# Optimization experiments

Measured on AMD Instinct MI355X. Metric: run time of the kernel, lower is better.

Reference implementation:

```python
import jax, jax.numpy as jnp
import numpy as np

B, L = 16, 512          # samples x tokens-per-sample
S = B * L               # total packed tokens
H, HKV, D = 16, 4, 128  # query heads, kv heads, head_dim
G = H // HKV            # GQA group size
HID = 2048
EPS = 1e-6


def rmsnorm(x, w):
    # Qwen2RMSNorm: fp32 variance, scale by weight
    v = jnp.mean(x.astype(jnp.float32) ** 2, axis=-1, keepdims=True)
    return (x.astype(jnp.float32) * jax.lax.rsqrt(v + EPS)).astype(x.dtype) * w


def rotate_half(x):
    x1, x2 = jnp.split(x, 2, axis=-1)
    return jnp.concatenate([-x2, x1], axis=-1)


def setup_inputs() -> dict:
    key = jax.random.key(0)
    ks = jax.random.split(key, 24)
    f = lambda k, shp, s=0.02: (jax.random.normal(k, shp, dtype=jnp.float32) * s)
    inp = {
        'packed_sequence_und': f(ks[0], (S // 2, HID), 1.0),
        'packed_sequence_gen': f(ks[1], (S // 2, HID), 1.0),
        # und tokens on even slots, gen on odd slots -> irregular scatter
        'packed_und_token_indexes': jnp.arange(0, S, 2, dtype=jnp.int32),
        'packed_gen_token_indexes': jnp.arange(1, S, 2, dtype=jnp.int32),
        # und-path projections (q/k/v have bias, o does not)
        'q_w': f(ks[2], (H * D, HID)), 'q_b': f(ks[3], (H * D,)),
        'k_w': f(ks[4], (HKV * D, HID)), 'k_b': f(ks[5], (HKV * D,)),
        'v_w': f(ks[6], (HKV * D, HID)), 'v_b': f(ks[7], (HKV * D,)),
        'o_w': f(ks[8], (HID, H * D)),
        # gen-path (moe_gen) projections
        'q_w_g': f(ks[9], (H * D, HID)), 'q_b_g': f(ks[10], (H * D,)),
        'k_w_g': f(ks[11], (HKV * D, HID)), 'k_b_g': f(ks[12], (HKV * D,)),
        'v_w_g': f(ks[13], (HKV * D, HID)), 'v_b_g': f(ks[14], (HKV * D,)),
        'o_w_g': f(ks[15], (HID, H * D)),
        # qk-norm weights
        'qn_w': jnp.ones((D,), jnp.float32), 'kn_w': jnp.ones((D,), jnp.float32),
        'qn_w_g': jnp.ones((D,), jnp.float32), 'kn_w_g': jnp.ones((D,), jnp.float32),
    }
    # RoPE cos/sin for packed positions (position resets per sample)
    pos = jnp.tile(jnp.arange(L, dtype=jnp.float32), B)            # [S]
    inv_freq = 1.0 / (1e6 ** (jnp.arange(0, D, 2, dtype=jnp.float32) / D))
    freqs = pos[:, None] * inv_freq[None, :]                       # [S, D/2]
    emb = jnp.concatenate([freqs, freqs], axis=-1)                 # [S, D]
    inp['packed_cos'] = jnp.cos(emb)
    inp['packed_sin'] = jnp.sin(emb)
    return inp


def reference(packed_sequence_und, packed_sequence_gen, packed_cos, packed_sin,
              packed_und_token_indexes, packed_gen_token_indexes,
              q_w, q_b, k_w, k_b, v_w, v_b, o_w,
              q_w_g, q_b_g, k_w_g, k_b_g, v_w_g, v_b_g, o_w_g,
              qn_w, kn_w, qn_w_g, kn_w_g):
    ui, gi = packed_und_token_indexes, packed_gen_token_indexes
    # dual-path QKV projection + index scatter into shared packed buffers
    q = jnp.zeros((S, H * D), jnp.float32)
    q = q.at[ui].set(packed_sequence_und @ q_w.T + q_b)
    q = q.at[gi].set(packed_sequence_gen @ q_w_g.T + q_b_g)
    k = jnp.zeros((S, HKV * D), jnp.float32)
    k = k.at[ui].set(packed_sequence_und @ k_w.T + k_b)
    k = k.at[gi].set(packed_sequence_gen @ k_w_g.T + k_b_g)
    v = jnp.zeros((S, HKV * D), jnp.float32)
    v = v.at[ui].set(packed_sequence_und @ v_w.T + v_b)
    v = v.at[gi].set(packed_sequence_gen @ v_w_g.T + v_b_g)

    q = q.reshape(S, H, D)
    k = k.reshape(S, HKV, D)
    v = v.reshape(S, HKV, D)

    # per-stream QK RMSNorm, scattered back
    q = jnp.zeros_like(q).at[ui].set(rmsnorm(q[ui], qn_w)).at[gi].set(rmsnorm(q[gi], qn_w_g))
    k = jnp.zeros_like(k).at[ui].set(rmsnorm(k[ui], kn_w)).at[gi].set(rmsnorm(k[gi], kn_w_g))

    # RoPE (unsqueeze_dim=1)
    cos, sin = packed_cos[:, None, :], packed_sin[:, None, :]
    q = q * cos + rotate_half(q) * sin
    k = k * cos + rotate_half(k) * sin

    # block-diagonal causal attention over packed samples (GQA)
    qb_ = q.reshape(B, L, HKV, G, D)
    kb_ = k.reshape(B, L, HKV, D)
    vb_ = v.reshape(B, L, HKV, D)
    scale = 1.0 / np.sqrt(D)
    scores = jnp.einsum('bqhgd,bkhd->bhgqk', qb_, kb_) * scale   # [B,HKV,G,L,L]
    causal = jnp.tril(jnp.ones((L, L), bool))
    scores = jnp.where(causal, scores, -jnp.inf)
    probs = jax.nn.softmax(scores, axis=-1)
    out = jnp.einsum('bhgqk,bkhd->bqhgd', probs, vb_)            # [B,L,HKV,G,D]
    out = out.reshape(S, H * D)

    out_und = out[ui] @ o_w.T
    out_gen = out[gi] @ o_w_g.T
    return (out_und, out_gen)
```

## Files before the change

### kernel.cpp

```cpp
#include <hip/hip_runtime.h>

typedef __bf16 bf16;
typedef __bf16 bf16x8 __attribute__((ext_vector_type(8)));
typedef float  f32x4  __attribute__((ext_vector_type(4)));

#define HALF   4096
#define S_TOT  8192
#define HID    2048
#define NH     16
#define NKV    4
#define DH     128
#define LSEQ   512

typedef const __attribute__((address_space(1))) void* as1_cvp;
typedef __attribute__((address_space(3))) void* as3_vp;

__device__ __forceinline__ void gl2lds16(const void* g, void* l) {
    __builtin_amdgcn_global_load_lds((as1_cvp)g, (as3_vp)l, 16, 0, 0);
}

struct CvtArgs {
    const float* src[10];
    bf16*        dst[10];
    int          n4[10];
};
__global__ __launch_bounds__(256) void k_convert_multi(CvtArgs a, int total4) {
    int i = blockIdx.x * 256 + threadIdx.x;
    if (i >= total4) return;
    int off = i;
    #pragma unroll
    for (int s = 0; s < 10; ++s) {
        if (off < a.n4[s]) {
            float4 v = ((const float4*)a.src[s])[off];
            union { bf16 b[4]; ushort4 u; } t;
            t.b[0] = (bf16)v.x; t.b[1] = (bf16)v.y; t.b[2] = (bf16)v.z; t.b[3] = (bf16)v.w;
            ((ushort4*)a.dst[s])[off] = t.u;
            return;
        }
        off -= a.n4[s];
    }
}

__global__ void k_invtyp(const int* __restrict__ ui, const int* __restrict__ gi,
                         int* __restrict__ it) {
    int t = blockIdx.x * 256 + threadIdx.x;
    if (t < HALF) { it[ui[t]] = t << 1; it[gi[t]] = (t << 1) | 1; }
}

__global__ __launch_bounds__(256) void k_gemm_qkv(
    const bf16* __restrict__ Xu, const bf16* __restrict__ Xg,
    const bf16* __restrict__ Wu, const bf16* __restrict__ Wg,
    const float* __restrict__ qbu, const float* __restrict__ kbu, const float* __restrict__ vbu,
    const float* __restrict__ qbg, const float* __restrict__ kbg, const float* __restrict__ vbg,
    const int* __restrict__ ui, const int* __restrict__ gi,
    bf16* __restrict__ qo, bf16* __restrict__ ko, bf16* __restrict__ vo)
{
    const int gen = blockIdx.z;
    const bf16* X = gen ? Xg : Xu;
    const bf16* W = gen ? Wg : Wu;
    const float* qb = gen ? qbg : qbu;
    const float* kb = gen ? kbg : kbu;
    const float* vb = gen ? vbg : vbu;
    const int* idx = gen ? gi : ui;

    __shared__ __align__(16) bf16 sA[128*32];
    __shared__ __align__(16) bf16 sB[128*32];

    const int tid = threadIdx.x;
    const int wave = tid >> 6, lane = tid & 63;
    const int lm = lane & 15, kq = lane >> 4;
    const int wm = wave >> 1, wn = wave & 1;
    const int m0 = blockIdx.y * 128, n0 = blockIdx.x * 128;

    f32x4 acc[4][4] = {};

    for (int k0 = 0; k0 < HID; k0 += 32) {
        __syncthreads();
        #pragma unroll
        for (int i = 0; i < 2; ++i) {
            const int g = i*4 + wave;
            const int c = g*64 + lane;
            const int row = c >> 2, col = c & 3;
            gl2lds16(X + (size_t)(m0+row)*HID + k0 + col*8, (char*)sA + (size_t)g*1024);
            gl2lds16(W + (size_t)(n0+row)*HID + k0 + col*8, (char*)sB + (size_t)g*1024);
        }
        __syncthreads();
        bf16x8 a[4], b[4];
        #pragma unroll
        for (int i = 0; i < 4; ++i) a[i] = *(const bf16x8*)&sA[(wm*64 + i*16 + lm)*32 + kq*8];
        #pragma unroll
        for (int j = 0; j < 4; ++j) b[j] = *(const bf16x8*)&sB[(wn*64 + j*16 + lm)*32 + kq*8];
        #pragma unroll
        for (int i = 0; i < 4; ++i)
            #pragma unroll
            for (int j = 0; j < 4; ++j)
                acc[i][j] = __builtin_amdgcn_mfma_f32_16x16x32_bf16(a[i], b[j], acc[i][j], 0, 0, 0);
    }

    #pragma unroll
    for (int i = 0; i < 4; ++i) {
        int srow[4];
        #pragma unroll
        for (int r = 0; r < 4; ++r) srow[r] = idx[m0 + wm*64 + i*16 + kq*4 + r];
        #pragma unroll
        for (int j = 0; j < 4; ++j) {
            const int o = n0 + wn*64 + j*16 + lm;
            bf16* dst; float bias; int off0, ld;
            if (o < 2048)      { dst = qo; ld = 2048; off0 = o;        bias = qb[o]; }
            else if (o < 2560) { dst = ko; ld = 512;  off0 = o - 2048; bias = kb[o-2048]; }
            else               { dst = vo; ld = 512;  off0 = o - 2560; bias = vb[o-2560]; }
            #pragma unroll
            for (int r = 0; r < 4; ++r)
                dst[(size_t)srow[r]*ld + off0] = (bf16)(acc[i][j][r] + bias);
        }
    }
}

__global__ __launch_bounds__(256) void k_norm_rope(
    bf16* __restrict__ qbuf, bf16* __restrict__ kbuf,
    const float* __restrict__ cosb, const float* __restrict__ sinb,
    const int* __restrict__ invtyp,
    const float* __restrict__ qnu, const float* __restrict__ qng,
    const float* __restrict__ knu, const float* __restrict__ kng)
{
    const int row = blockIdx.x * 4 + (threadIdx.x >> 6);
    const int lane = threadIdx.x & 63;
    const int s = row / (NH + NKV), hh = row % (NH + NKV);
    const int isg = invtyp[s] & 1;
    bf16* ptr; const float* w; float qs;
    if (hh < NH) { ptr = qbuf + (size_t)s*HID + hh*DH;           w = isg ? qng : qnu;
                   qs = 0.08838834764831845f * 1.4426950408889634f; }
    else         { ptr = kbuf + (size_t)s*(NKV*DH) + (hh-NH)*DH; w = isg ? kng : knu;
                   qs = 1.0f; }

    const unsigned u = *(const unsigned*)((const unsigned short*)ptr + 2*lane);
    const float f0 = __uint_as_float(u << 16);
    const float f1 = __uint_as_float(u & 0xffff0000u);
    float ss = f0*f0 + f1*f1;
    #pragma unroll
    for (int m = 32; m; m >>= 1) ss += __shfl_xor(ss, m, 64);
    const float r = rsqrtf(ss * (1.0f/128.0f) + 1e-6f);
    const float2 wv = *(const float2*)(w + 2*lane);
    const float xn0 = f0 * r * wv.x;
    const float xn1 = f1 * r * wv.y;
    const float po0 = __shfl_xor(xn0, 32, 64);
    const float po1 = __shfl_xor(xn1, 32, 64);
    const float2 c2 = *(const float2*)(cosb + (size_t)s*DH + 2*lane);
    const float2 s2 = *(const float2*)(sinb + (size_t)s*DH + 2*lane);
    const float sg = (lane < 32) ? -1.0f : 1.0f;
    const float o0 = (xn0 * c2.x + sg * po0 * s2.x) * qs;
    const float o1 = (xn1 * c2.y + sg * po1 * s2.y) * qs;
    union { unsigned short us[2]; unsigned u; } t;
    bf16 b0 = (bf16)o0, b1 = (bf16)o1;
    t.us[0] = *(unsigned short*)&b0; t.us[1] = *(unsigned short*)&b1;
    *(unsigned*)((unsigned short*)ptr + 2*lane) = t.u;
}

__global__ __launch_bounds__(256) void k_vtrans(const bf16* __restrict__ v, bf16* __restrict__ vt)
{
    __shared__ __align__(16) bf16 sT[64 * 132];
    const int kvh = blockIdx.y;
    const int s0 = blockIdx.x * 64;
    const int b = s0 >> 9;
    const int pos0 = s0 & 511;
    const int tid = threadIdx.x;

    #pragma unroll
    for (int i = 0; i < 4; ++i) {
        const int c = i*256 + tid;
        const int rowi = c >> 4, col8 = c & 15;
        const uint4 d = *(const uint4*)(v + (size_t)(s0 + rowi)*(NKV*DH) + kvh*DH + col8*8);
        uint2* lp = (uint2*)&sT[rowi*132 + col8*8];
        lp[0] = make_uint2(d.x, d.y);
        lp[1] = make_uint2(d.z, d.w);
    }
    __syncthreads();
    const int dd = tid >> 1, half = tid & 1;
    __align__(16) bf16 tmp[32];
    #pragma unroll
    for (int p = 0; p < 32; ++p) tmp[p] = sT[(half*32 + p)*132 + dd];
    bf16* dst = vt + ((size_t)(b*NKV + kvh)*DH + dd)*LSEQ + pos0 + half*32;
    #pragma unroll
    for (int q = 0; q < 8; ++q) ((ushort4*)dst)[q] = ((ushort4*)tmp)[q];
}

__global__ __launch_bounds__(256) void k_attn(
    const bf16* __restrict__ qbuf, const bf16* __restrict__ kbuf,
    const bf16* __restrict__ vt, const int* __restrict__ invtyp,
    bf16* __restrict__ aop_u, bf16* __restrict__ aop_g)
{
    __shared__ __align__(16) bf16 sK[2][64*128];
    __shared__ __align__(16) bf16 sV[2][128*64];
    __shared__ __align__(16) bf16 sP[4][16*72];

    const int qt = 7 - blockIdx.x;
    const int h = blockIdx.y, b = blockIdx.z;
    const int kvh = h >> 2;
    const int tid = threadIdx.x, wave = tid >> 6, lane = tid & 63;
    const int lm = lane & 15, kq = lane >> 4;
    const int q0 = qt * 64;

    bf16x8 qfrag[4];
    {
        const bf16* qp = qbuf + ((size_t)(b*LSEQ + q0 + wave*16 + lm))*HID + h*DH;
        #pragma unroll
        for (int ks = 0; ks < 4; ++ks)
            qfrag[ks] = *(const bf16x8*)(qp + ks*32 + kq*8);
    }

    const bf16* kbase = kbuf + ((size_t)(b*LSEQ))*(NKV*DH) + kvh*DH;
    const bf16* vbase = vt + ((size_t)(b*NKV + kvh)*DH)*LSEQ;

    f32x4 accO[8] = {};
    float lpart[4] = {0.f, 0.f, 0.f, 0.f};
    bf16* const sPw = &sP[wave][0];

    {
        const bf16* kp = kbase;
        const bf16* vp = vbase;
        #pragma unroll
        for (int i = 0; i < 4; ++i) {
            const int g = i*4 + wave;
            const int ch = g*64 + lane;
            { const int row = ch >> 4, cp = ch & 15;
              const int c = (cp & 8) | ((cp ^ row) & 7);
              gl2lds16(kp + (size_t)row*(NKV*DH) + c*8, (char*)&sK[0][0] + (size_t)g*1024); }
            { const int d = ch >> 3, cp = ch & 7;
              const int c = (cp ^ d) & 7;
              gl2lds16(vp + (size_t)d*LSEQ + c*8, (char*)&sV[0][0] + (size_t)g*1024); }
        }
    }

    for (int kt = 0; kt <= qt; ++kt) {
        const int cur = kt & 1;
        __syncthreads();

        if (kt < qt) {
            const bf16* kp = kbase + (size_t)((kt+1)*64)*(NKV*DH);
            const bf16* vp = vbase + (kt+1)*64;
            const int nxt = cur ^ 1;
            #pragma unroll
            for (int i = 0; i < 4; ++i) {
                const int g = i*4 + wave;
                const int ch = g*64 + lane;
                { const int row = ch >> 4, cp = ch & 15;
                  const int c = (cp & 8) | ((cp ^ row) & 7);
                  gl2lds16(kp + (size_t)row*(NKV*DH) + c*8, (char*)&sK[nxt][0] + (size_t)g*1024); }
                { const int d = ch >> 3, cp = ch & 7;
                  const int c = (cp ^ d) & 7;
                  gl2lds16(vp + (size_t)d*LSEQ + c*8, (char*)&sV[nxt][0] + (size_t)g*1024); }
            }
        }

        f32x4 s4[4] = {};
        #pragma unroll
        for (int ks = 0; ks < 4; ++ks) {
            const int cq = ks*4 + kq;
            const int cs = (cq & 8) | ((cq ^ lm) & 7);
            #pragma unroll
            for (int nt = 0; nt < 4; ++nt) {
                bf16x8 bk = *(const bf16x8*)&sK[cur][(nt*16 + lm)*128 + cs*8];
                s4[nt] = __builtin_amdgcn_mfma_f32_16x16x32_bf16(qfrag[ks], bk, s4[nt], 0, 0, 0);
            }
        }

        const bool diag = (kt == qt);
        #pragma unroll
        for (int r = 0; r < 4; ++r) {
            const int rloc = wave*16 + kq*4 + r;
            float v0 = s4[0][r], v1 = s4[1][r], v2 = s4[2][r], v3 = s4[3][r];
            if (diag) {
                if (lm      > rloc) v0 = -1e30f;
                if (lm + 16 > rloc) v1 = -1e30f;
                if (lm + 32 > rloc) v2 = -1e30f;
                if (lm + 48 > rloc) v3 = -1e30f;
            }
            const float p0 = exp2f(v0);
            const float p1 = exp2f(v1);
            const float p2 = exp2f(v2);
            const float p3 = exp2f(v3);
            lpart[r] += (p0 + p1) + (p2 + p3);
            const int prow = (kq*4 + r) * 72;
            sPw[prow + lm]      = (bf16)p0;
            sPw[prow + 16 + lm] = (bf16)p1;
            sPw[prow + 32 + lm] = (bf16)p2;
            sPw[prow + 48 + lm] = (bf16)p3;
        }

        #pragma unroll
        for (int pc = 0; pc < 2; ++pc) {
            bf16x8 ap = *(const bf16x8*)&sPw[lm*72 + pc*32 + kq*8];
            #pragma unroll
            for (int dt = 0; dt < 8; ++dt) {
                const int cv = (pc*4 + kq);
                const int cs = (cv ^ lm) & 7;
                bf16x8 bv = *(const bf16x8*)&sV[cur][(dt*16 + lm)*64 + cs*8];
                accO[dt] = __builtin_amdgcn_mfma_f32_16x16x32_bf16(ap, bv, accO[dt], 0, 0, 0);
            }
        }
    }

    #pragma unroll
    for (int r = 0; r < 4; ++r) {
        float l = lpart[r];
        l += __shfl_xor(l, 1, 64);
        l += __shfl_xor(l, 2, 64);
        l += __shfl_xor(l, 4, 64);
        l += __shfl_xor(l, 8, 64);
        const int srow = b*LSEQ + q0 + wave*16 + kq*4 + r;
        const int code = invtyp[srow];
        bf16* dst = (code & 1) ? aop_g : aop_u;
        const size_t off = (size_t)(code >> 1)*HID + h*DH;
        const float inv_l = 1.0f / l;
        #pragma unroll
        for (int dt = 0; dt < 8; ++dt)
            dst[off + dt*16 + lm] = (bf16)(accO[dt][r] * inv_l);
    }
}

__global__ __launch_bounds__(256) void k_gemm_out(
    const bf16* __restrict__ Au, const bf16* __restrict__ Ag,
    const bf16* __restrict__ Wu, const bf16* __restrict__ Wg,
    float* __restrict__ out)
{
    const int gen = blockIdx.z;
    const bf16* A = gen ? Ag : Au;
    const bf16* W = gen ? Wg : Wu;
    float* O = out + (size_t)gen * HALF * HID;

    __shared__ __align__(16) bf16 sA[128*32];
    __shared__ __align__(16) bf16 sB[128*32];

    const int tid = threadIdx.x;
    const int wave = tid >> 6, lane = tid & 63;
    const int lm = lane & 15, kq = lane >> 4;
    const int wm = wave >> 1, wn = wave & 1;
    const int m0 = blockIdx.y * 128, n0 = blockIdx.x * 128;

    f32x4 acc[4][4] = {};

    for (int k0 = 0; k0 < HID; k0 += 32) {
        __syncthreads();
        #pragma unroll
        for (int i = 0; i < 2; ++i) {
            const int g = i*4 + wave;
            const int c = g*64 + lane;
            const int row = c >> 2, col = c & 3;
            gl2lds16(A + (size_t)(m0+row)*HID + k0 + col*8, (char*)sA + (size_t)g*1024);
            gl2lds16(W + (size_t)(n0+row)*HID + k0 + col*8, (char*)sB + (size_t)g*1024);
        }
        __syncthreads();
        bf16x8 a[4], b[4];
        #pragma unroll
        for (int i = 0; i < 4; ++i) a[i] = *(const bf16x8*)&sA[(wm*64 + i*16 + lm)*32 + kq*8];
        #pragma unroll
        for (int j = 0; j < 4; ++j) b[j] = *(const bf16x8*)&sB[(wn*64 + j*16 + lm)*32 + kq*8];
        #pragma unroll
        for (int i = 0; i < 4; ++i)
            #pragma unroll
            for (int j = 0; j < 4; ++j)
                acc[i][j] = __builtin_amdgcn_mfma_f32_16x16x32_bf16(a[i], b[j], acc[i][j], 0, 0, 0);
    }

    #pragma unroll
    for (int i = 0; i < 4; ++i)
        #pragma unroll
        for (int j = 0; j < 4; ++j)
            #pragma unroll
            for (int r = 0; r < 4; ++r)
                O[(size_t)(m0 + wm*64 + i*16 + kq*4 + r)*HID + (n0 + wn*64 + j*16 + lm)] = acc[i][j][r];
}

extern "C" void kernel_launch(void* const* d_in, const int* in_sizes, int n_in,
                              void* d_out, int out_size, void* d_ws, size_t ws_size,
                              hipStream_t stream)
{
    (void)in_sizes; (void)n_in; (void)out_size; (void)ws_size;
    const float* x_u  = (const float*)d_in[0];
    const float* x_g  = (const float*)d_in[1];
    const int*   ui   = (const int*)d_in[2];
    const int*   gi   = (const int*)d_in[3];
    const float* q_w  = (const float*)d_in[4];
    const float* q_b  = (const float*)d_in[5];
    const float* k_w  = (const float*)d_in[6];
    const float* k_b  = (const float*)d_in[7];
    const float* v_w  = (const float*)d_in[8];
    const float* v_b  = (const float*)d_in[9];
    const float* o_w  = (const float*)d_in[10];
    const float* q_wg = (const float*)d_in[11];
    const float* q_bg = (const float*)d_in[12];
    const float* k_wg = (const float*)d_in[13];
    const float* k_bg = (const float*)d_in[14];
    const float* v_wg = (const float*)d_in[15];
    const float* v_bg = (const float*)d_in[16];
    const float* o_wg = (const float*)d_in[17];
    const float* qn_u = (const float*)d_in[18];
    const float* kn_u = (const float*)d_in[19];
    const float* qn_g = (const float*)d_in[20];
    const float* kn_g = (const float*)d_in[21];
    const float* cosb = (const float*)d_in[22];
    const float* sinb = (const float*)d_in[23];

    char* w = (char*)d_ws;
    auto alloc = [&](size_t bytes) { char* p = w; w += (bytes + 255) & ~(size_t)255; return p; };
    bf16* xb_u   = (bf16*)alloc((size_t)HALF*HID*2);
    bf16* xb_g   = (bf16*)alloc((size_t)HALF*HID*2);
    bf16* wqkv_u = (bf16*)alloc((size_t)3072*HID*2);
    bf16* wqkv_g = (bf16*)alloc((size_t)3072*HID*2);
    bf16* wo_u   = (bf16*)alloc((size_t)HID*HID*2);
    bf16* wo_g   = (bf16*)alloc((size_t)HID*HID*2);
    bf16* qbuf   = (bf16*)alloc((size_t)S_TOT*HID*2);
    bf16* kbuf   = (bf16*)alloc((size_t)S_TOT*NKV*DH*2);
    bf16* vbuf   = (bf16*)alloc((size_t)S_TOT*NKV*DH*2);
    bf16* vtb    = (bf16*)alloc((size_t)S_TOT*NKV*DH*2);
    int*  invtyp = (int*)alloc((size_t)S_TOT*4);
    bf16* aop_u = xb_u;
    bf16* aop_g = xb_g;

    CvtArgs ca;
    int total4 = 0, si = 0;
    auto seg = [&](const float* s, bf16* d, size_t n) {
        ca.src[si] = s; ca.dst[si] = d; ca.n4[si] = (int)(n / 4);
        total4 += (int)(n / 4); ++si;
    };
    seg(x_u,  xb_u,                (size_t)HALF*HID);
    seg(x_g,  xb_g,                (size_t)HALF*HID);
    seg(q_w,  wqkv_u,              (size_t)2048*HID);
    seg(k_w,  wqkv_u + 2048*HID,   (size_t)512*HID);
    seg(v_w,  wqkv_u + 2560*HID,   (size_t)512*HID);
    seg(q_wg, wqkv_g,              (size_t)2048*HID);
    seg(k_wg, wqkv_g + 2048*HID,   (size_t)512*HID);
    seg(v_wg, wqkv_g + 2560*HID,   (size_t)512*HID);
    seg(o_w,  wo_u,                (size_t)HID*HID);
    seg(o_wg, wo_g,                (size_t)HID*HID);
    k_convert_multi<<<(total4 + 255)/256, 256, 0, stream>>>(ca, total4);

    k_invtyp<<<16, 256, 0, stream>>>(ui, gi, invtyp);

    k_gemm_qkv<<<dim3(24, 32, 2), 256, 0, stream>>>(
        xb_u, xb_g, wqkv_u, wqkv_g,
        q_b, k_b, v_b, q_bg, k_bg, v_bg,
        ui, gi, qbuf, kbuf, vbuf);

    k_norm_rope<<<(S_TOT*(NH+NKV))/4, 256, 0, stream>>>(
        qbuf, kbuf, cosb, sinb, invtyp, qn_u, qn_g, kn_u, kn_g);

    k_vtrans<<<dim3(S_TOT/64, NKV), 256, 0, stream>>>(vbuf, vtb);

    k_attn<<<dim3(LSEQ/64, NH, 16), 256, 0, stream>>>(
        qbuf, kbuf, vtb, invtyp, aop_u, aop_g);

    k_gemm_out<<<dim3(16, 32, 2), 256, 0, stream>>>(
        aop_u, aop_g, wo_u, wo_g, (float*)d_out);
}
```

Before: 565.2 us.

## Rewrite QKV and output GEMMs as 256x256 multi-buffered pipelined tiles

Both projection GEMMs now share a 256x256-tile, 512-thread core that stages global-to-LDS loads several k-chunks ahead into a double-buffered, XOR-swizzled shared-memory layout. Explicit barriers, vmcnt waits and MFMA priority raising are meant to overlap loads with matrix math. This removes the per-k-step full synchronisation and bank conflicts of the old 128x128 single-buffer loop and raises data reuse per tile. In exchange it uses 128KB of LDS per block, which is more LDS and register pressure, and it launches far fewer blocks (384 and 256).

```diff
diff --git a/kernel.cpp b/kernel.cpp
--- a/kernel.cpp
+++ b/kernel.cpp
@@ -18,6 +18,13 @@
 __device__ __forceinline__ void gl2lds16(const void* g, void* l) {
     __builtin_amdgcn_global_load_lds((as1_cvp)g, (as3_vp)l, 16, 0, 0);
 }
+
+__device__ __forceinline__ void hard_barrier() {
+    __builtin_amdgcn_sched_barrier(0);
+    __builtin_amdgcn_s_barrier();
+    __builtin_amdgcn_sched_barrier(0);
+}
+#define VMCNT(n) asm volatile("s_waitcnt vmcnt(" #n ")" ::: "memory")
 
 struct CvtArgs {
     const float* src[10];
@@ -47,7 +54,102 @@
     if (t < HALF) { it[ui[t]] = t << 1; it[gi[t]] = (t << 1) | 1; }
 }
 
-__global__ __launch_bounds__(256) void k_gemm_qkv(
+__device__ __forceinline__ void stage_chunk(const bf16* __restrict__ g,
+    int row0, int kcol, char* chunk, int tid)
+{
+    const int wave = tid >> 6;
+    #pragma unroll
+    for (int j = 0; j < 2; ++j) {
+        const int sidx = j*512 + tid;
+        const int row  = sidx >> 2;
+        const int csw  = (sidx & 3) ^ ((row >> 1) & 3);
+        gl2lds16(g + (size_t)(row0 + row)*HID + kcol + csw*8,
+                 chunk + (size_t)(j*512 + wave*64)*16);
+    }
+}
+
+#define PHASE(BUF, MH, KH, STG, TAIL)                                           \
+  {                                                                             \
+    const char* Ab_ = sAb + (BUF)*32768 + (KH)*16384;                           \
+    const char* Bb_ = sBb + (BUF)*32768 + (KH)*16384;                           \
+    bf16x8 af_[4], bf_[4];                                                      \
+    _Pragma("unroll")                                                           \
+    for (int im = 0; im < 4; ++im)                                              \
+        af_[im] = *(const bf16x8*)(Ab_ + aoff[MH][im]);                         \
+    _Pragma("unroll")                                                           \
+    for (int jn = 0; jn < 4; ++jn)                                              \
+        bf_[jn] = *(const bf16x8*)(Bb_ + boff[jn]);                             \
+    STG;                                                                        \
+    hard_barrier();                                                             \
+    __builtin_amdgcn_s_setprio(1);                                              \
+    _Pragma("unroll")                                                           \
+    for (int im = 0; im < 4; ++im)                                              \
+      _Pragma("unroll")                                                         \
+      for (int jn = 0; jn < 4; ++jn)                                            \
+        acc[(MH)*4+im][jn] = __builtin_amdgcn_mfma_f32_16x16x32_bf16(           \
+            af_[im], bf_[jn], acc[(MH)*4+im][jn], 0, 0, 0);                     \
+    __builtin_amdgcn_s_setprio(0);                                              \
+    TAIL;                                                                       \
+    hard_barrier();                                                             \
+  }
+
+__device__ __forceinline__ void gemm256_core(
+    const bf16* __restrict__ A, const bf16* __restrict__ B,
+    int m0, int n0, int tid, char* sAb, char* sBb, f32x4 (&acc)[8][4])
+{
+    const int lane = tid & 63;
+    const int lm = lane & 15, kq = lane >> 4;
+    const int wave = tid >> 6;
+    const int wm = wave >> 2, wn = wave & 3;
+
+    int aoff[2][4]; int boff[4];
+    #pragma unroll
+    for (int mh = 0; mh < 2; ++mh)
+        #pragma unroll
+        for (int im = 0; im < 4; ++im) {
+            const int row = wm*128 + mh*64 + im*16 + lm;
+            aoff[mh][im] = row*64 + ((kq ^ ((row >> 1) & 3)) * 16);
+        }
+    #pragma unroll
+    for (int jn = 0; jn < 4; ++jn) {
+        const int row = wn*64 + jn*16 + lm;
+        boff[jn] = row*64 + ((kq ^ ((row >> 1) & 3)) * 16);
+    }
+
+    stage_chunk(A, m0, 0,  sAb + 0,     tid);
+    stage_chunk(A, m0, 32, sAb + 16384, tid);
+    stage_chunk(B, n0, 0,  sBb + 0,     tid);
+    stage_chunk(B, n0, 32, sBb + 16384, tid);
+    stage_chunk(A, m0, 64, sAb + 32768, tid);
+    stage_chunk(B, n0, 64, sBb + 32768, tid);
+    VMCNT(4);
+    hard_barrier();
+
+    #pragma unroll 1
+    for (int i = 0; i < 15; ++i) {
+        const int t1k = (2*i+1)*64, t2k = (2*i+2)*64, t3k = (2*i+3)*64;
+        PHASE(0,0,0, stage_chunk(A, m0, t1k+32, sAb + 49152, tid), (void)0);
+        PHASE(0,1,0, stage_chunk(B, n0, t1k+32, sBb + 49152, tid), (void)0);
+        PHASE(0,0,1, stage_chunk(A, m0, t2k,    sAb + 0,     tid), (void)0);
+        PHASE(0,1,1, stage_chunk(B, n0, t2k,    sBb + 0,     tid), VMCNT(4));
+        PHASE(1,0,0, stage_chunk(A, m0, t2k+32, sAb + 16384, tid), (void)0);
+        PHASE(1,1,0, stage_chunk(B, n0, t2k+32, sBb + 16384, tid), (void)0);
+        PHASE(1,0,1, stage_chunk(A, m0, t3k,    sAb + 32768, tid), (void)0);
+        PHASE(1,1,1, stage_chunk(B, n0, t3k,    sBb + 32768, tid), VMCNT(4));
+    }
+    {
+        PHASE(0,0,0, stage_chunk(A, m0, 2016, sAb + 49152, tid), (void)0);
+        PHASE(0,1,0, stage_chunk(B, n0, 2016, sBb + 49152, tid), (void)0);
+        PHASE(0,0,1, (void)0, (void)0);
+        PHASE(0,1,1, (void)0, VMCNT(0));
+        PHASE(1,0,0, (void)0, (void)0);
+        PHASE(1,1,0, (void)0, (void)0);
+        PHASE(1,0,1, (void)0, (void)0);
+        PHASE(1,1,1, (void)0, (void)0);
+    }
+}
+
+__global__ __launch_bounds__(512, 2) void k_gemm_qkv(
     const bf16* __restrict__ Xu, const bf16* __restrict__ Xg,
     const bf16* __restrict__ Wu, const bf16* __restrict__ Wg,
     const float* __restrict__ qbu, const float* __restrict__ kbu, const float* __restrict__ vbu,
@@ -55,6 +157,9 @@
     const int* __restrict__ ui, const int* __restrict__ gi,
     bf16* __restrict__ qo, bf16* __restrict__ ko, bf16* __restrict__ vo)
 {
+    __shared__ __align__(16) bf16 sA[2][2][256*32];
+    __shared__ __align__(16) bf16 sB[2][2][256*32];
+
     const int gen = blockIdx.z;
     const bf16* X = gen ? Xg : Xu;
     const bf16* W = gen ? Wg : Wu;
@@ -63,55 +168,30 @@
     const float* vb = gen ? vbg : vbu;
     const int* idx = gen ? gi : ui;
 
-    __shared__ __align__(16) bf16 sA[128*32];
-    __shared__ __align__(16) bf16 sB[128*32];
-
     const int tid = threadIdx.x;
     const int wave = tid >> 6, lane = tid & 63;
     const int lm = lane & 15, kq = lane >> 4;
-    const int wm = wave >> 1, wn = wave & 1;
-    const int m0 = blockIdx.y * 128, n0 = blockIdx.x * 128;
-
-    f32x4 acc[4][4] = {};
-
-    for (int k0 = 0; k0 < HID; k0 += 32) {
-        __syncthreads();
-        #pragma unroll
-        for (int i = 0; i < 2; ++i) {
-            const int g = i*4 + wave;
-            const int c = g*64 + lane;
-            const int row = c >> 2, col = c & 3;
-            gl2lds16(X + (size_t)(m0+row)*HID + k0 + col*8, (char*)sA + (size_t)g*1024);
-            gl2lds16(W + (size_t)(n0+row)*HID + k0 + col*8, (char*)sB + (size_t)g*1024);
-        }
-        __syncthreads();
-        bf16x8 a[4], b[4];
-        #pragma unroll
-        for (int i = 0; i < 4; ++i) a[i] = *(const bf16x8*)&sA[(wm*64 + i*16 + lm)*32 + kq*8];
-        #pragma unroll
-        for (int j = 0; j < 4; ++j) b[j] = *(const bf16x8*)&sB[(wn*64 + j*16 + lm)*32 + kq*8];
-        #pragma unroll
-        for (int i = 0; i < 4; ++i)
-            #pragma unroll
-            for (int j = 0; j < 4; ++j)
-                acc[i][j] = __builtin_amdgcn_mfma_f32_16x16x32_bf16(a[i], b[j], acc[i][j], 0, 0, 0);
-    }
-
-    #pragma unroll
-    for (int i = 0; i < 4; ++i) {
+    const int wm = wave >> 2, wn = wave & 3;
+    const int m0 = blockIdx.y * 256, n0 = blockIdx.x * 256;
+
+    f32x4 acc[8][4] = {};
+    gemm256_core(X, W, m0, n0, tid, (char*)&sA[0][0][0], (char*)&sB[0][0][0], acc);
+
+    #pragma unroll
+    for (int im = 0; im < 8; ++im) {
         int srow[4];
         #pragma unroll
-        for (int r = 0; r < 4; ++r) srow[r] = idx[m0 + wm*64 + i*16 + kq*4 + r];
-        #pragma unroll
-        for (int j = 0; j < 4; ++j) {
-            const int o = n0 + wn*64 + j*16 + lm;
+        for (int r = 0; r < 4; ++r) srow[r] = idx[m0 + wm*128 + im*16 + kq*4 + r];
+        #pragma unroll
+        for (int jn = 0; jn < 4; ++jn) {
+            const int o = n0 + wn*64 + jn*16 + lm;
             bf16* dst; float bias; int off0, ld;
             if (o < 2048)      { dst = qo; ld = 2048; off0 = o;        bias = qb[o]; }
             else if (o < 2560) { dst = ko; ld = 512;  off0 = o - 2048; bias = kb[o-2048]; }
             else               { dst = vo; ld = 512;  off0 = o - 2560; bias = vb[o-2560]; }
             #pragma unroll
             for (int r = 0; r < 4; ++r)
-                dst[(size_t)srow[r]*ld + off0] = (bf16)(acc[i][j][r] + bias);
+                dst[(size_t)srow[r]*ld + off0] = (bf16)(acc[im][jn][r] + bias);
         }
     }
 }
@@ -318,57 +398,36 @@
     }
 }
 
-__global__ __launch_bounds__(256) void k_gemm_out(
+__global__ __launch_bounds__(512, 2) void k_gemm_out(
     const bf16* __restrict__ Au, const bf16* __restrict__ Ag,
     const bf16* __restrict__ Wu, const bf16* __restrict__ Wg,
     float* __restrict__ out)
 {
+    __shared__ __align__(16) bf16 sA[2][2][256*32];
+    __shared__ __align__(16) bf16 sB[2][2][256*32];
+
     const int gen = blockIdx.z;
     const bf16* A = gen ? Ag : Au;
     const bf16* W = gen ? Wg : Wu;
     float* O = out + (size_t)gen * HALF * HID;
 
-    __shared__ __align__(16) bf16 sA[128*32];
-    __shared__ __align__(16) bf16 sB[128*32];
-
     const int tid = threadIdx.x;
     const int wave = tid >> 6, lane = tid & 63;
     const int lm = lane & 15, kq = lane >> 4;
-    const int wm = wave >> 1, wn = wave & 1;
-    const int m0 = blockIdx.y * 128, n0 = blockIdx.x * 128;
-
-    f32x4 acc[4][4] = {};
-
-    for (int k0 = 0; k0 < HID; k0 += 32) {
-        __syncthreads();
-        #pragma unroll
-        for (int i = 0; i < 2; ++i) {
-            const int g = i*4 + wave;
-            const int c = g*64 + lane;
-            const int row = c >> 2, col = c & 3;
-            gl2lds16(A + (size_t)(m0+row)*HID + k0 + col*8, (char*)sA + (size_t)g*1024);
-            gl2lds16(W + (size_t)(n0+row)*HID + k0 + col*8, (char*)sB + (size_t)g*1024);
-        }
-        __syncthreads();
-        bf16x8 a[4], b[4];
-        #pragma unroll
-        for (int i = 0; i < 4; ++i) a[i] = *(const bf16x8*)&sA[(wm*64 + i*16 + lm)*32 + kq*8];
-        #pragma unroll
-        for (int j = 0; j < 4; ++j) b[j] = *(const bf16x8*)&sB[(wn*64 + j*16 + lm)*32 + kq*8];
-        #pragma unroll
-        for (int i = 0; i < 4; ++i)
-            #pragma unroll
-            for (int j = 0; j < 4; ++j)
-                acc[i][j] = __builtin_amdgcn_mfma_f32_16x16x32_bf16(a[i], b[j], acc[i][j], 0, 0, 0);
-    }
-
-    #pragma unroll
-    for (int i = 0; i < 4; ++i)
-        #pragma unroll
-        for (int j = 0; j < 4; ++j)
+    const int wm = wave >> 2, wn = wave & 3;
+    const int m0 = blockIdx.y * 256, n0 = blockIdx.x * 256;
+
+    f32x4 acc[8][4] = {};
+    gemm256_core(A, W, m0, n0, tid, (char*)&sA[0][0][0], (char*)&sB[0][0][0], acc);
+
+    #pragma unroll
+    for (int im = 0; im < 8; ++im)
+        #pragma unroll
+        for (int jn = 0; jn < 4; ++jn)
             #pragma unroll
             for (int r = 0; r < 4; ++r)
-                O[(size_t)(m0 + wm*64 + i*16 + kq*4 + r)*HID + (n0 + wn*64 + j*16 + lm)] = acc[i][j][r];
+                O[(size_t)(m0 + wm*128 + im*16 + kq*4 + r)*HID + (n0 + wn*64 + jn*16 + lm)]
+                    = acc[im][jn][r];
 }
 
 extern "C" void kernel_launch(void* const* d_in, const int* in_sizes, int n_in,
@@ -437,7 +496,7 @@
 
     k_invtyp<<<16, 256, 0, stream>>>(ui, gi, invtyp);
 
-    k_gemm_qkv<<<dim3(24, 32, 2), 256, 0, stream>>>(
+    k_gemm_qkv<<<dim3(12, 16, 2), 512, 0, stream>>>(
         xb_u, xb_g, wqkv_u, wqkv_g,
         q_b, k_b, v_b, q_bg, k_bg, v_bg,
         ui, gi, qbuf, kbuf, vbuf);
@@ -450,6 +509,6 @@
     k_attn<<<dim3(LSEQ/64, NH, 16), 256, 0, stream>>>(
         qbuf, kbuf, vtb, invtyp, aop_u, aop_g);
 
-    k_gemm_out<<<dim3(16, 32, 2), 256, 0, stream>>>(
+    k_gemm_out<<<dim3(8, 16, 2), 512, 0, stream>>>(
         aop_u, aop_g, wo_u, wo_g, (float*)d_out);
 }
```

Measured after the change: 542.7 us. 1.04x faster.
